# Optimization experiments

Measured on AMD Instinct MI355X. Metric: run time of the kernel, lower is better.

The kernel has to match this reference:

```python
import jax, jax.numpy as jnp
import numpy as np

D = 64            # packed days (admission nodes)
VD = 4525         # drug vocab per day
VL = 753          # labitem vocab per day
ND, NLN = D * VD, D * VL
H = 128           # h_dim
EMB = 10          # embedding_size
TV = 100          # token-field vocab size
NH, HD = 8, 16    # attention heads, head dim
L_ENC, FF = 6, 2048
GL = 2            # gnn layers
ED, ET = 32768, 131072  # did / took edge counts
K = 256           # candidates per day


def setup_inputs():
    key = jax.random.key(0)
    ks = iter(jax.random.split(key, 80))
    nk = lambda: next(ks)
    w = lambda *s: 0.02 * jax.random.normal(nk(), s, jnp.float32)
    ones_zeros = jnp.tile(jnp.stack([jnp.ones(H), jnp.zeros(H)])[None], (L_ENC, 1, 1))
    inp = {
        'drug_tokens': jax.random.randint(nk(), (ND, 3), 0, TV),
        'drug_node_id': jax.random.randint(nk(), (ND,), 0, VD),
        'drug_floats': jax.random.normal(nk(), (ND, 2), jnp.float32),
        'lab_tokens': jax.random.randint(nk(), (NLN, 2), 0, TV),
        'lab_node_id': jax.random.randint(nk(), (NLN,), 0, VL),
        'lab_floats': jax.random.normal(nk(), (NLN, 1), jnp.float32),
        'adm_tokens': jax.random.randint(nk(), (D, 4), 0, TV),
        'adm_floats': jax.random.normal(nk(), (D, 3), jnp.float32),
        'did_tokens': jax.random.randint(nk(), (ED, 2), 0, TV),
        'did_floats': jax.random.normal(nk(), (ED, 2), jnp.float32),
        'did_src': jax.random.randint(nk(), (ED,), 0, D),
        'did_dst': jax.random.randint(nk(), (ED,), 0, NLN),
        'took_tokens': jax.random.randint(nk(), (ET, 2), 0, TV),
        'took_floats': jax.random.normal(nk(), (ET, 1), jnp.float32),
        'took_src': jax.random.randint(nk(), (ET,), 0, D),
        'took_dst': jax.random.randint(nk(), (ET,), 0, ND),
        'cand_idx': jax.random.randint(nk(), (D - 1, K), 0, VD),
        # learned parameters (normal std=0.02 as in _init_weights)
        'drug_id_emb': w(VD, EMB), 'lab_id_emb': w(VL, EMB),
        'drug_tok_emb': w(3, TV, EMB), 'lab_tok_emb': w(2, TV, EMB),
        'adm_tok_emb': w(4, TV, EMB),
        'did_tok_emb': w(2, TV, EMB), 'took_tok_emb': w(2, TV, EMB),
        'drug_float_w': w(2, EMB), 'lab_float_w': w(1, EMB), 'adm_float_w': w(3, EMB),
        'did_float_w': w(2, EMB), 'took_float_w': w(1, EMB),
        'drug_align': w(5 * EMB, H), 'lab_align': w(4 * EMB, H), 'adm_align': w(5 * EMB, H),
        'did_align': w(3 * EMB, H), 'took_align': w(3 * EMB, H),
        'gnn_w_msg': w(GL, 4, H, H), 'gnn_w_self': w(GL, 3, H, H),
        'tr_qkv_w': w(L_ENC, H, 3 * H), 'tr_qkv_b': jnp.zeros((L_ENC, 3 * H), jnp.float32),
        'tr_out_w': w(L_ENC, H, H), 'tr_out_b': jnp.zeros((L_ENC, H), jnp.float32),
        'tr_ln1': ones_zeros,
        'tr_ff1_w': w(L_ENC, H, FF), 'tr_ff1_b': jnp.zeros((L_ENC, FF), jnp.float32),
        'tr_ff2_w': w(L_ENC, FF, H), 'tr_ff2_b': jnp.zeros((L_ENC, H), jnp.float32),
        'tr_ln2': ones_zeros,
        'lp_w': w(H),
    }
    return inp


def _graph_embed(tokens, floats, tok_emb, float_w):
    # per-field token embedding lookup + one slot from float fields -> [N, n_tok+1, EMB]
    nf = tok_emb.shape[0]
    te = tok_emb[jnp.arange(nf), tokens]
    fe = (floats @ float_w)[:, None, :]
    return jnp.concatenate([te, fe], axis=1)


def _seg_mean(msgs, idx, n):
    s = jax.ops.segment_sum(msgs, idx, num_segments=n)
    c = jax.ops.segment_sum(jnp.ones((msgs.shape[0],), msgs.dtype), idx, num_segments=n)
    return s / jnp.maximum(c, 1.0)[:, None]


def _ln(x, sb):
    mu = x.mean(-1, keepdims=True)
    var = ((x - mu) ** 2).mean(-1, keepdims=True)
    return sb[0] * (x - mu) * jax.lax.rsqrt(var + 1e-5) + sb[1]


def _forward(fl, it):
    (drug_floats, lab_floats, adm_floats, did_floats, took_floats,
     drug_id_emb, lab_id_emb, drug_tok_emb, lab_tok_emb, adm_tok_emb,
     did_tok_emb, took_tok_emb, drug_float_w, lab_float_w, adm_float_w,
     did_float_w, took_float_w, drug_align, lab_align, adm_align,
     did_align, took_align, gnn_w_msg, gnn_w_self,
     tr_qkv_w, tr_qkv_b, tr_out_w, tr_out_b, tr_ln1,
     tr_ff1_w, tr_ff1_b, tr_ff2_w, tr_ff2_b, tr_ln2, lp_w) = fl
    (drug_tokens, drug_node_id, lab_tokens, lab_node_id, adm_tokens,
     did_tokens, took_tokens, did_src, did_dst, took_src, took_dst, cand_idx) = it
    # per-type embed + concat(id, fields) + align (LazyLinear, no bias)
    x_d = jnp.concatenate([drug_id_emb[drug_node_id][:, None, :],
                           _graph_embed(drug_tokens, drug_floats, drug_tok_emb, drug_float_w)], 1)
    x_d = x_d.reshape(ND, -1) @ drug_align
    x_l = jnp.concatenate([lab_id_emb[lab_node_id][:, None, :],
                           _graph_embed(lab_tokens, lab_floats, lab_tok_emb, lab_float_w)], 1)
    x_l = x_l.reshape(NLN, -1) @ lab_align
    x_a = _graph_embed(adm_tokens, adm_floats, adm_tok_emb, adm_float_w).reshape(D, -1) @ adm_align
    e_did = _graph_embed(did_tokens, did_floats, did_tok_emb, did_float_w).reshape(ED, -1) @ did_align
    e_took = _graph_embed(took_tokens, took_floats, took_tok_emb, took_float_w).reshape(ET, -1) @ took_align
    # hetero message passing (to_hetero: per-edge-type conv, sum over incoming types)
    for l in range(GL):
        m_l = _seg_mean((x_a[did_src] + e_did) @ gnn_w_msg[l, 0], did_dst, NLN)
        m_d = _seg_mean((x_a[took_src] + e_took) @ gnn_w_msg[l, 1], took_dst, ND)
        m_a = (_seg_mean((x_l[did_dst] + e_did) @ gnn_w_msg[l, 2], did_src, D)
               + _seg_mean((x_d[took_dst] + e_took) @ gnn_w_msg[l, 3], took_src, D))
        x_a = x_a @ gnn_w_self[l, 0] + m_a
        x_d = x_d @ gnn_w_self[l, 1] + m_d
        x_l = x_l @ gnn_w_self[l, 2] + m_l
        if l < GL - 1:
            x_a, x_d, x_l = jax.nn.relu(x_a), jax.nn.relu(x_d), jax.nn.relu(x_l)
    # causal transformer encoder over per-day admission states (torch post-LN, relu)
    mask = jnp.where(jnp.tril(jnp.ones((D, D), bool)), 0.0, -1e9)
    h = x_a
    for i in range(L_ENC):
        q, k, v = jnp.split(h @ tr_qkv_w[i] + tr_qkv_b[i], 3, axis=-1)
        q = q.reshape(D, NH, HD); k = k.reshape(D, NH, HD); v = v.reshape(D, NH, HD)
        att = jax.nn.softmax(jnp.einsum('qhd,khd->hqk', q, k) * 0.25 + mask, axis=-1)
        o = jnp.einsum('hqk,khd->qhd', att, v).reshape(D, H) @ tr_out_w[i] + tr_out_b[i]
        h = _ln(h + o, tr_ln1[i])
        f = jax.nn.relu(h @ tr_ff1_w[i] + tr_ff1_b[i]) @ tr_ff2_w[i] + tr_ff2_b[i]
        h = _ln(h + f, tr_ln2[i])
    # link prediction: prev-day patient state vs candidate item embeddings
    drug_day = x_d.reshape(D, VD, H)
    items = drug_day[jnp.arange(D - 1)[:, None], cand_idx]  # [D-1, K, H]
    logits = jnp.einsum('dkh,dh,h->dk', items, h[:D - 1], lp_w)
    return logits


def reference(drug_floats, lab_floats, adm_floats, did_floats, took_floats,
              drug_id_emb, lab_id_emb, drug_tok_emb, lab_tok_emb, adm_tok_emb,
              did_tok_emb, took_tok_emb, drug_float_w, lab_float_w, adm_float_w,
              did_float_w, took_float_w, drug_align, lab_align, adm_align,
              did_align, took_align, gnn_w_msg, gnn_w_self,
              tr_qkv_w, tr_qkv_b, tr_out_w, tr_out_b, tr_ln1,
              tr_ff1_w, tr_ff1_b, tr_ff2_w, tr_ff2_b, tr_ln2, lp_w,
              drug_tokens, drug_node_id, lab_tokens, lab_node_id, adm_tokens,
              did_tokens, took_tokens, did_src, did_dst, took_src, took_dst, cand_idx):
    fl = (drug_floats, lab_floats, adm_floats, did_floats, took_floats,
          drug_id_emb, lab_id_emb, drug_tok_emb, lab_tok_emb, adm_tok_emb,
          did_tok_emb, took_tok_emb, drug_float_w, lab_float_w, adm_float_w,
          did_float_w, took_float_w, drug_align, lab_align, adm_align,
          did_align, took_align, gnn_w_msg, gnn_w_self,
          tr_qkv_w, tr_qkv_b, tr_out_w, tr_out_b, tr_ln1,
          tr_ff1_w, tr_ff1_b, tr_ff2_w, tr_ff2_b, tr_ln2, lp_w)
    it = (drug_tokens, drug_node_id, lab_tokens, lab_node_id, adm_tokens,
          did_tokens, took_tokens, did_src, did_dst, took_src, took_dst, cand_idx)
    return _forward(fl, it)
```

## Files before the change

### kernel.cpp

```cpp
#include <hip/hip_runtime.h>
#include <hip/hip_bf16.h>

typedef unsigned short ushort_t;
typedef unsigned long long u64;
typedef __attribute__((ext_vector_type(8))) short bf16x8;
typedef __attribute__((ext_vector_type(4))) float f32x4;

#define DEV __device__ __forceinline__

constexpr int Dd  = 64;
constexpr int VD  = 4525;
constexpr int VL  = 753;
constexpr int ND  = Dd * VD;
constexpr int NLN = Dd * VL;
constexpr int Hh  = 128;
constexpr int EMB = 10;
constexpr int TV  = 100;
constexpr int NH  = 8, HD = 16;
constexpr int L_ENC = 6, FF = 2048;
constexpr int GL  = 2;
constexpr int ED  = 32768, ET = 131072;
constexpr int KK  = 256;
constexpr int NCAND = (Dd - 1) * KK;
constexpr int UCAP  = ET + NCAND;
// ... 16 lines not shown
{
    int tid = threadIdx.x;
    int c = 0;
    #pragma unroll
    for (int i = 0; i < 16; i++) c += (w[tid * 16 + i] >> 14) & 1;
    #pragma unroll
    for (int o = 32; o; o >>= 1) c += __shfl_xor(c, o);
    if (tid == 0) *flag = (c > 256) ? 1 : 0;
}

struct CanonDesc {
    const void* src[NCANON];
    int doff[NCANON];
    int bend[NCANON];
    int n[NCANON];
};

__global__ __launch_bounds__(256)
void k_canon(CanonDesc cd, float* __restrict__ dst, const int* __restrict__ flag)
{
    int b = blockIdx.x;
    int t = 0;
    while (t < NCANON && b >= cd.bend[t]) t++;
    if (t >= NCANON) return;
    int bstart = (t == 0) ? 0 : cd.bend[t - 1];
    int i = (b - bstart) * 256 + threadIdx.x;
    if (i >= cd.n[t]) return;
    float v = (*flag) ? ((const float*)cd.src[t])[i]
                      : bf(((const ushort_t*)cd.src[t])[i]);
    dst[cd.doff[t] + i] = v;
}

__global__ __launch_bounds__(128)
void k_wpack(const float* __restrict__ gself, const float* __restrict__ gmsg,
             ushort_t* __restrict__ wt)
{
    const int selfIdx[3] = {1, 2, 4};
    const int msgIdx[3]  = {1, 0, 5};
    int pr = blockIdx.y, chunk = blockIdx.x, nn = threadIdx.x;
    const float* Ws = gself + (size_t)selfIdx[pr] * Hh * Hh;
    const float* Wm = gmsg  + (size_t)msgIdx[pr]  * Hh * Hh;
    ushort_t* dst = wt + (((size_t)pr * 32 + chunk) * 128 + nn) * 8;
    #pragma unroll
    for (int j = 0; j < 8; j++) {
        int k = chunk * 8 + j;
        float v = (k < 128) ? Ws[k * Hh + nn] : Wm[(k - 128) * Hh + nn];
        dst[j] = f2bf(v);
    }
}

__global__ __launch_bounds__(128)
void k_apack(const float* __restrict__ A, ushort_t* __restrict__ dst, int L)
{
    int c = blockIdx.x, nn = threadIdx.x;
    ushort_t* d = dst + ((size_t)c * 128 + nn) * 8;
    #pragma unroll
    for (int j = 0; j < 8; j++) {
        int k = c * 8 + j;
        d[j] = (k < L) ? f2bf(A[(size_t)k * Hh + nn]) : (ushort_t)0;
    }
}

__global__ __launch_bounds__(256)
void k_mark(const int* __restrict__ took_dst, const int* __restrict__ cand,
            int* __restrict__ map)
{
    int g = blockIdx.x * 256 + threadIdx.x;
    if (g < ET) atomicOr(&map[took_dst[g]], 1);
    if (g < NCAND) {
        int d = g >> 8;
        atomicOr(&map[d * VD + cand[g]], 2);
    }
}

__global__ __launch_bounds__(256)
void k_acount(const int* __restrict__ map, u64* __restrict__ bsum)
{
    __shared__ u64 s[256];
    int tid = threadIdx.x;
    int g = blockIdx.x * 256 + tid;
    int m = (g < ND) ? map[g] : 0;
    s[tid] = (u64)(m ? 1u : 0u) | ((u64)((m & 2) ? 1u : 0u) << 32);
    __syncthreads();
    for (int o = 128; o; o >>= 1) {
        if (tid < o) s[tid] += s[tid + o];
        __syncthreads();
    }
    if (tid == 0) bsum[blockIdx.x] = s[0];
}

__global__ __launch_bounds__(1024)
void k_ascan(u64* __restrict__ bsum, int nb, int* __restrict__ nUB)
// ... 50 lines not shown
}

__global__ __launch_bounds__(256)
void k_counts(const int* __restrict__ did_dst, const int* __restrict__ did_src,
              const int* __restrict__ took_dst, const int* __restrict__ took_src,
              const int* __restrict__ map,
              int* __restrict__ cnt_ld, int* __restrict__ cnt_a1,
              int* __restrict__ cnt_dc, int* __restrict__ cnt_a2)
{
    __shared__ int h1[64], h2[64];
    int tid = threadIdx.x;
    if (tid < 64) { h1[tid] = 0; h2[tid] = 0; }
    __syncthreads();
    int tb = blockIdx.x * 1024;
    #pragma unroll
    for (int o = 0; o < 1024; o += 256) {
        int i = tb + o + tid;
        atomicAdd(&cnt_dc[map[took_dst[i]] >> 2], 1);
        atomicAdd(&h2[took_src[i]], 1);
    }
    {
        int i = blockIdx.x * 256 + tid;
        atomicAdd(&cnt_ld[did_dst[i]], 1);
        atomicAdd(&h1[did_src[i]], 1);
    }
    __syncthreads();
    if (tid < 64) {
        if (h1[tid]) atomicAdd(&cnt_a1[tid], h1[tid]);
        if (h2[tid]) atomicAdd(&cnt_a2[tid], h2[tid]);
    }
}

__global__ __launch_bounds__(256)
void k_scan_blk(const int* __restrict__ cnt, int* __restrict__ excl,
                int* __restrict__ btot, int n)
{
    __shared__ int s[256];
    int tid = threadIdx.x;
    int g = blockIdx.x * 256 + tid;
    int v = (g < n) ? cnt[g] : 0;
    s[tid] = v;
    __syncthreads();
    for (int o = 1; o < 256; o <<= 1) {
        int t = (tid >= o) ? s[tid - o] : 0;
        __syncthreads();
        s[tid] += t;
        __syncthreads();
    }
    if (g < n) excl[g] = s[tid] - v;
    if (tid == 255) btot[blockIdx.x] = s[255];
}

__global__ __launch_bounds__(1024)
void k_scan_top(int* __restrict__ btot, int nb)
{
    __shared__ int s[1024];
    int tid = threadIdx.x;
    int v = (tid < nb) ? btot[tid] : 0;
    s[tid] = v;
    __syncthreads();
    for (int o = 1; o < 1024; o <<= 1) {
        int t = (tid >= o) ? s[tid - o] : 0;
        __syncthreads();
        s[tid] += t;
        __syncthreads();
    }
    if (tid < nb) btot[tid] = s[tid] - v;
}

__global__ __launch_bounds__(256)
void k_scan_add(int* __restrict__ roff, const int* __restrict__ btot, int n, int total)
{
    int g = blockIdx.x * 256 + threadIdx.x;
    if (g < n) roff[g] += btot[blockIdx.x];
    if (g == 0) roff[n] = total;
}

__global__ __launch_bounds__(64)
void k_scan64(const int* __restrict__ c1, const int* __restrict__ c2,
              int* __restrict__ r1, int* __restrict__ r2)
{
    int tid = threadIdx.x;
    int v1 = c1[tid], v2 = c2[tid];
    int s1 = v1, s2 = v2;
    for (int o = 1; o < 64; o <<= 1) {
        int t1 = __shfl_up(s1, o), t2 = __shfl_up(s2, o);
        if (tid >= o) { s1 += t1; s2 += t2; }
    }
    r1[tid] = s1 - v1;
    r2[tid] = s2 - v2;
}

__global__ __launch_bounds__(256)
void k_fill(const int* __restrict__ did_src, const int* __restrict__ did_dst,
            const int* __restrict__ took_src, const int* __restrict__ took_dst,
            const int* __restrict__ map,
            const int* __restrict__ roff_d, const int* __restrict__ roff_t,
            const int* __restrict__ roff_a1, const int* __restrict__ roff_a2,
            int* __restrict__ cur_d, int* __restrict__ cur_t,
            int* __restrict__ cur_a1, int* __restrict__ cur_a2,
            int* __restrict__ elist_d, int* __restrict__ elist_t,
            int* __restrict__ didA, int* __restrict__ didB,
            int* __restrict__ tookA, int* __restrict__ tookB)
{
    __shared__ int h1[64], h2[64], b1[64], b2[64];
    int tid = threadIdx.x;
    if (tid < 64) { h1[tid] = 0; h2[tid] = 0; }
    __syncthreads();
    int tb = blockIdx.x * 1024;
    int db = blockIdx.x * 256;
    #pragma unroll
    for (int o = 0; o < 1024; o += 256)
        atomicAdd(&h2[took_src[tb + o + tid]], 1);
    atomicAdd(&h1[did_src[db + tid]], 1);
    __syncthreads();
    if (tid < 64) {
        b1[tid] = h1[tid] ? atomicAdd(&cur_a1[tid], h1[tid]) : 0;
        b2[tid] = h2[tid] ? atomicAdd(&cur_a2[tid], h2[tid]) : 0;
        h1[tid] = 0; h2[tid] = 0;
    }
    __syncthreads();
    #pragma unroll
    for (int o = 0; o < 1024; o += 256) {
// ... 163 lines not shown
    }
    __syncthreads();
    float* Ds = reinterpret_cast<float*>(As);
    #pragma unroll
    for (int nt = 0; nt < 8; nt++)
        #pragma unroll
        for (int reg = 0; reg < 4; reg++)
            Ds[(16 * wid + quad * 4 + reg) * 132 + nt * 16 + m] = acc[nt][reg];
    __syncthreads();
    for (int idx = tid; idx < 512; idx += 128) {
        int r = idx >> 4, c16 = idx & 15;
        int slot = r0 + r;
        if (slot >= n) continue;
        const float* dsrc = &Ds[r * 132 + c16 * 8];
        uint4 v;
        v.x = (unsigned)f2bf(dsrc[0]) | ((unsigned)f2bf(dsrc[1]) << 16);
        v.y = (unsigned)f2bf(dsrc[2]) | ((unsigned)f2bf(dsrc[3]) << 16);
        v.z = (unsigned)f2bf(dsrc[4]) | ((unsigned)f2bf(dsrc[5]) << 16);
        v.w = (unsigned)f2bf(dsrc[6]) | ((unsigned)f2bf(dsrc[7]) << 16);
        *reinterpret_cast<uint4*>(out + (size_t)slot * Hh + c16 * 8) = v;
    }
}

template<bool INDIRECT>
__global__ __launch_bounds__(128)
void k_gup(ushort_t* __restrict__ X, const float* __restrict__ xa,
           const ushort_t* __restrict__ ef,
           const int* __restrict__ roff, const int* __restrict__ elist, int sshift,
           const int* __restrict__ rows_list, const int* __restrict__ n_dyn, int n_static,
           const ushort_t* __restrict__ Wt, int do_relu)
{
    __shared__ ushort_t As[32 * 264];
    __shared__ int rowid[32];
    int tid = threadIdx.x;
    int r0 = blockIdx.x * 32;
    int n = n_dyn ? *n_dyn : n_static;
    if (tid < 32) {
        int row = r0 + tid;
        rowid[tid] = (row < n) ? (INDIRECT ? rows_list[row] : row) : -1;
    }
    __syncthreads();

    for (int idx = tid; idx < 512; idx += 128) {
        int r = idx >> 4, c16 = idx & 15;
        int rr = rowid[r];
        uint4 v = make_uint4(0, 0, 0, 0);
        if (rr >= 0) v = *reinterpret_cast<const uint4*>(X + (size_t)rr * Hh + c16 * 8);
        *reinterpret_cast<uint4*>(&As[r * 264 + c16 * 8]) = v;
    }
    int wid = tid >> 6, lane = tid & 63;
    int c0 = lane * 2;
    int emask = (1 << sshift) - 1;
    for (int r = wid; r < 32; r += 2) {
        int rr = rowid[r];
        float a0 = 0.f, a1 = 0.f, invd = 0.f;
        if (rr >= 0) {
            int e0 = roff[rr], e1 = roff[rr + 1];
            invd = 1.f / fmaxf((float)(e1 - e0), 1.f);
            for (int ei = e0; ei < e1; ei++) {
                int pk = elist[ei];
                int s = pk >> sshift, e = pk & emask;
                const float* xr = xa + s * Hh + c0;
                unsigned ee = *reinterpret_cast<const unsigned*>(ef + (size_t)e * Hh + c0);
                a0 += xr[0] + bflo(ee);
                a1 += xr[1] + bfhi(ee);
            }
        }
        unsigned pk2 = (unsigned)f2bf(a0 * invd) | ((unsigned)f2bf(a1 * invd) << 16);
        *reinterpret_cast<unsigned*>(&As[r * 264 + 128 + c0]) = pk2;
    }
    __syncthreads();

    int m = lane & 15, quad = lane >> 4;
    f32x4 acc[8];
    #pragma unroll
    for (int t = 0; t < 8; t++) acc[t] = (f32x4){0.f, 0.f, 0.f, 0.f};
    #pragma unroll
    for (int kc = 0; kc < 8; kc++) {
        bf16x8 a = *reinterpret_cast<const bf16x8*>(&As[(16 * wid + m) * 264 + kc * 32 + quad * 8]);
        #pragma unroll
        for (int nt = 0; nt < 8; nt++) {
            bf16x8 b = *reinterpret_cast<const bf16x8*>(Wt + (((kc * 4 + quad) * 128) + nt * 16 + m) * 8);
            acc[nt] = __builtin_amdgcn_mfma_f32_16x16x32_bf16(a, b, acc[nt], 0, 0, 0);
        }
    }
    __syncthreads();
    float* Ds = reinterpret_cast<float*>(As);
    #pragma unroll
    for (int nt = 0; nt < 8; nt++)
        #pragma unroll
        for (int reg = 0; reg < 4; reg++)
            Ds[(16 * wid + quad * 4 + reg) * 132 + nt * 16 + m] = acc[nt][reg];
    __syncthreads();
// ... 13 lines not shown
        v.y = (unsigned)f2bf(o[2]) | ((unsigned)f2bf(o[3]) << 16);
        v.z = (unsigned)f2bf(o[4]) | ((unsigned)f2bf(o[5]) << 16);
        v.w = (unsigned)f2bf(o[6]) | ((unsigned)f2bf(o[7]) << 16);
        *reinterpret_cast<uint4*>(X + (size_t)rr * Hh + c16 * 8) = v;
    }
}

__global__ __launch_bounds__(128)
void k_xa(float* __restrict__ x_a,
          const float* __restrict__ Sx1, const float* __restrict__ E1,
          const float* __restrict__ Sx2, const float* __restrict__ E2,
          const int* __restrict__ c1, const int* __restrict__ c2,
          const float* __restrict__ Wself, const float* __restrict__ Wm1,
          const float* __restrict__ Wm2, int do_relu)
{
    int r = blockIdx.x, tid = threadIdx.x;
    __shared__ float xr[128], a1[128], a2[128];
    float i1 = 1.f / fmaxf((float)c1[r], 1.f);
    float i2 = 1.f / fmaxf((float)c2[r], 1.f);
    xr[tid] = x_a[r * Hh + tid];
    a1[tid] = (Sx1[r * Hh + tid] + E1[r * Hh + tid]) * i1;
    a2[tid] = (Sx2[r * Hh + tid] + E2[r * Hh + tid]) * i2;
    __syncthreads();
    float acc = 0.f;
    for (int k = 0; k < 128; k++) {
        acc = fmaf(xr[k], Wself[k * Hh + tid], acc);
        acc = fmaf(a1[k], Wm1[k * Hh + tid], acc);
        acc = fmaf(a2[k], Wm2[k * Hh + tid], acc);
    }
    if (do_relu) acc = fmaxf(acc, 0.f);
    x_a[r * Hh + tid] = acc;
}

__global__ __launch_bounds__(128)
void k_qkv3(const float* __restrict__ h, float* __restrict__ qkv,
            const float* __restrict__ W, const float* __restrict__ b)
{
    int r = blockIdx.x, part = blockIdx.y, tid = threadIdx.x;
    int c = part * 128 + tid;
    __shared__ float hr[128];
    hr[tid] = h[r * Hh + tid];
    __syncthreads();
    float a0 = b[c], a1 = 0.f, a2 = 0.f, a3 = 0.f;
    for (int k = 0; k < 128; k += 4) {
        a0 = fmaf(hr[k],     W[(k)     * 384 + c], a0);
        a1 = fmaf(hr[k + 1], W[(k + 1) * 384 + c], a1);
        a2 = fmaf(hr[k + 2], W[(k + 2) * 384 + c], a2);
        a3 = fmaf(hr[k + 3], W[(k + 3) * 384 + c], a3);
    }
    qkv[r * 384 + c] = (a0 + a1) + (a2 + a3);
}

__global__ __launch_bounds__(64)
void k_attn2(const float* __restrict__ qkv, float* __restrict__ attn_o)
{
    int hh = blockIdx.x, q = blockIdx.y;
    int lane = threadIdx.x;
    const float* qv = qkv + q * 384 + hh * HD;
    const float* kv = qkv + lane * 384 + 128 + hh * HD;
    float s = 0.f;
    #pragma unroll
    for (int d2 = 0; d2 < HD; d2++) s = fmaf(qv[d2], kv[d2], s);
    s = s * 0.25f + (lane <= q ? 0.f : -1e9f);
    float m = s;
    #pragma unroll
    for (int o = 32; o; o >>= 1) m = fmaxf(m, __shfl_xor(m, o));
    float e = __expf(s - m);
    float tot = e;
    #pragma unroll
    for (int o = 32; o; o >>= 1) tot += __shfl_xor(tot, o);
    float att = e / tot;
    __shared__ float satt[64];
    satt[lane] = att;
    __syncthreads();
    if (lane < HD) {
        float o0 = 0.f, o1 = 0.f, o2 = 0.f, o3 = 0.f;
        for (int k2 = 0; k2 < Dd; k2 += 4) {
            o0 = fmaf(satt[k2],     qkv[(k2)     * 384 + 256 + hh * HD + lane], o0);
            o1 = fmaf(satt[k2 + 1], qkv[(k2 + 1) * 384 + 256 + hh * HD + lane], o1);
            o2 = fmaf(satt[k2 + 2], qkv[(k2 + 2) * 384 + 256 + hh * HD + lane], o2);
            o3 = fmaf(satt[k2 + 3], qkv[(k2 + 3) * 384 + 256 + hh * HD + lane], o3);
        }
        attn_o[q * Hh + hh * HD + lane] = (o0 + o1) + (o2 + o3);
    }
}

DEV float blocksum128(float v, float* red)
{
    #pragma unroll
    for (int o = 32; o; o >>= 1) v += __shfl_xor(v, o);
    int wid = threadIdx.x >> 6;
    __syncthreads();
    if ((threadIdx.x & 63) == 0) red[wid] = v;
    __syncthreads();
    return red[0] + red[1];
}

__global__ __launch_bounds__(128)
void k_outln(const float* __restrict__ attn_o, float* __restrict__ h,
             const float* __restrict__ Wout, const float* __restrict__ bout,
             const float* __restrict__ ln)
{
    int r = blockIdx.x, tid = threadIdx.x;
    __shared__ float ar[128];
    __shared__ float red[2];
    ar[tid] = attn_o[r * Hh + tid];
    __syncthreads();
    float a0 = bout[tid], a1 = 0.f, a2 = 0.f, a3 = 0.f;
    for (int k = 0; k < 128; k += 4) {
        a0 = fmaf(ar[k],     Wout[(k)     * Hh + tid], a0);
        a1 = fmaf(ar[k + 1], Wout[(k + 1) * Hh + tid], a1);
        a2 = fmaf(ar[k + 2], Wout[(k + 2) * Hh + tid], a2);
        a3 = fmaf(ar[k + 3], Wout[(k + 3) * Hh + tid], a3);
    }
    float x = h[r * Hh + tid] + (a0 + a1) + (a2 + a3);
    float mu = blocksum128(x, red) * (1.f / 128.f);
    float dx = x - mu;
    float var = blocksum128(dx * dx, red) * (1.f / 128.f);
    h[r * Hh + tid] = ln[tid] * dx * (1.f / sqrtf(var + 1e-5f)) + ln[128 + tid];
}

__global__ __launch_bounds__(256)
void k_ff1b(const float* __restrict__ h, float* __restrict__ fbuf,
            const float* __restrict__ W1, const float* __restrict__ b1)
{
    int r = blockIdx.x, tid = threadIdx.x;
    int c = blockIdx.y * 256 + tid;
    __shared__ float hr[128];
    if (tid < 128) hr[tid] = h[r * Hh + tid];
    __syncthreads();
    float a0 = b1[c], a1 = 0.f, a2 = 0.f, a3 = 0.f;
    for (int k = 0; k < 128; k += 4) {
        a0 = fmaf(hr[k],     W1[(size_t)(k)     * FF + c], a0);
        a1 = fmaf(hr[k + 1], W1[(size_t)(k + 1) * FF + c], a1);
        a2 = fmaf(hr[k + 2], W1[(size_t)(k + 2) * FF + c], a2);
        a3 = fmaf(hr[k + 3], W1[(size_t)(k + 3) * FF + c], a3);
    }
    fbuf[(size_t)r * FF + c] = fmaxf((a0 + a1) + (a2 + a3), 0.f);
}

__global__ __launch_bounds__(128)
void k_ff2p(const float* __restrict__ fbuf, float* __restrict__ part,
            const float* __restrict__ W2)
{
    int r = blockIdx.x, pi = blockIdx.y, tid = threadIdx.x;
    int kc = pi * 128;
    const float* f = fbuf + (size_t)r * FF + kc;
    float a0 = 0.f, a1 = 0.f, a2 = 0.f, a3 = 0.f;
    for (int k = 0; k < 128; k += 4) {
        a0 = fmaf(f[k],     W2[(size_t)(kc + k)     * Hh + tid], a0);
        a1 = fmaf(f[k + 1], W2[(size_t)(kc + k + 1) * Hh + tid], a1);
        a2 = fmaf(f[k + 2], W2[(size_t)(kc + k + 2) * Hh + tid], a2);
        a3 = fmaf(f[k + 3], W2[(size_t)(kc + k + 3) * Hh + tid], a3);
    }
    part[(size_t)(r * 16 + pi) * Hh + tid] = (a0 + a1) + (a2 + a3);
}

__global__ __launch_bounds__(128)
void k_ln2(float* __restrict__ h, const float* __restrict__ part,
           const float* __restrict__ b2, const float* __restrict__ ln)
{
    int r = blockIdx.x, tid = threadIdx.x;
    __shared__ float red[2];
    float acc = b2[tid];
    #pragma unroll
    for (int pi = 0; pi < 16; pi++) acc += part[(size_t)(r * 16 + pi) * Hh + tid];
    float x = h[r * Hh + tid] + acc;
    float mu = blocksum128(x, red) * (1.f / 128.f);
    float dx = x - mu;
    float var = blocksum128(dx * dx, red) * (1.f / 128.f);
    h[r * Hh + tid] = ln[tid] * dx * (1.f / sqrtf(var + 1e-5f)) + ln[128 + tid];
}

__global__ __launch_bounds__(256)
void k_logits(const ushort_t* __restrict__ x_dc, const int* __restrict__ map,
              const float* __restrict__ h, const float* __restrict__ lp,
              const int* __restrict__ cand, float* __restrict__ out)
{
    int d = blockIdx.x;
    int tid = threadIdx.x, lane = tid & 63, w = tid >> 6;
    __shared__ float wv[128];
    if (tid < 128) wv[tid] = h[d * Hh + tid] * lp[tid];
    __syncthreads();
    for (int k = w; k < KK; k += 4) {
        int slot = map[d * VD + cand[d * KK + k]] >> 2;
        const ushort_t* row = x_dc + (size_t)slot * Hh;
        float v = bf(row[lane]) * wv[lane] + bf(row[lane + 64]) * wv[lane + 64];
        #pragma unroll
// ... 44 lines not shown
            cd.doff[t] = e;
            e = (e + cn[t] + 7) & ~7;
            btot_blocks += (cn[t] + 255) / 256;
            cd.bend[t] = btot_blocks;
        }
        eoff[NCANON] = e;
    }

    char* p = (char*)d_ws;
    auto alloc_f = [&](size_t n) -> float*    { float* r = (float*)p;    p += n * sizeof(float); return r; };
    auto alloc_h = [&](size_t n) -> ushort_t* { ushort_t* r = (ushort_t*)p; p += n * sizeof(ushort_t); return r; };
    auto alloc_i = [&](size_t n) -> int*      { int* r = (int*)p;        p += n * sizeof(int); return r; };

    int* map    = alloc_i(ND);
    int* cnt_dc = alloc_i(UCAP);
    int* cnt_ld = alloc_i(NLN);
    int* cnt_a1 = alloc_i(64);
    int* cnt_a2 = alloc_i(64);
    int* nUB    = alloc_i(8);
    int* cur_t  = alloc_i(UCAP);
    int* cur_d  = alloc_i(NLN);
    int* cur_a1 = alloc_i(64);
    int* cur_a2 = alloc_i(64);
    float* E_did  = alloc_f((size_t)Dd * Hh);
    float* E_took = alloc_f((size_t)Dd * Hh);
    const size_t ZBLOCK = (size_t)ND + UCAP + NLN + 64 + 64 + 8 + UCAP + NLN + 64 + 64
                        + (size_t)Dd * Hh * 2;
    float* Sx_did  = alloc_f((size_t)Dd * Hh);
    float* Sx_took = alloc_f((size_t)Dd * Hh);
    int* roff_t  = alloc_i(UCAP + 8);
    int* roff_d  = alloc_i(NLN + 8);
    int* roff_a1 = alloc_i(72);
    int* roff_a2 = alloc_i(72);
    int* bscr    = alloc_i(1024);
    u64* absum   = (u64*)alloc_i(2 * (NB_A + 8));
    int* ulist   = alloc_i(UCAP);
    int* blist   = alloc_i(NCAND);
    int* elist_t = alloc_i(ET);
    int* elist_d = alloc_i(ED);
    int* tookA   = alloc_i(ET);
    int* tookB   = alloc_i(ET);
    int* didA    = alloc_i(ED);
    int* didB    = alloc_i(ED);
    ushort_t* wt     = alloc_h(3 * 32768);
    ushort_t* ap     = alloc_h(2 * 8192 + 2 * 4096);
    ushort_t* x_dc   = alloc_h((size_t)UCAP * Hh);
    ushort_t* x_l    = alloc_h((size_t)NLN * Hh);
    float*    x_a    = alloc_f((size_t)Dd * Hh);
    ushort_t* e_did  = alloc_h((size_t)ED * Hh);
    ushort_t* e_took = alloc_h((size_t)ET * Hh);
    float*    qkvb   = alloc_f((size_t)Dd * 384);
    float*    attn_o = alloc_f((size_t)Dd * Hh);
    float*    fbuf   = alloc_f((size_t)Dd * FF);
    float*    part   = alloc_f((size_t)Dd * 16 * Hh);
    float*    cf     = alloc_f((size_t)eoff[NCANON]);
    int*      dflag  = alloc_i(8);

    ushort_t* ap_drug = ap;
    ushort_t* ap_lab  = ap + 8192;
    ushort_t* ap_did  = ap + 16384;
    ushort_t* ap_took = ap + 16384 + 4096;

    const float* c_drug_floats  = cf + eoff[0];
    const float* c_lab_floats   = cf + eoff[1];
    const float* c_adm_floats   = cf + eoff[2];
    const float* c_did_floats   = cf + eoff[3];
    const float* c_took_floats  = cf + eoff[4];
    const float* c_drug_id_emb  = cf + eoff[5];
    const float* c_lab_id_emb   = cf + eoff[6];
    const float* c_drug_tok_emb = cf + eoff[7];
    const float* c_lab_tok_emb  = cf + eoff[8];
    const float* c_adm_tok_emb  = cf + eoff[9];
    const float* c_did_tok_emb  = cf + eoff[10];
    const float* c_took_tok_emb = cf + eoff[11];
    const float* c_drug_float_w = cf + eoff[12];
    const float* c_lab_float_w  = cf + eoff[13];
    const float* c_adm_float_w  = cf + eoff[14];
    const float* c_did_float_w  = cf + eoff[15];
    const float* c_took_float_w = cf + eoff[16];
    const float* c_drug_align   = cf + eoff[17];
    const float* c_lab_align    = cf + eoff[18];
    const float* c_adm_align    = cf + eoff[19];
    const float* c_did_align    = cf + eoff[20];
    const float* c_took_align   = cf + eoff[21];
    const float* c_gnn_msg      = cf + eoff[22];
    const float* c_gnn_self     = cf + eoff[23];
    const float* c_qkv_w        = cf + eoff[24];
    const float* c_qkv_b        = cf + eoff[25];
    const float* c_out_w        = cf + eoff[26];
    const float* c_out_b        = cf + eoff[27];
    const float* c_ln1          = cf + eoff[28];
    const float* c_ff1_w        = cf + eoff[29];
    const float* c_ff1_b        = cf + eoff[30];
    const float* c_ff2_w        = cf + eoff[31];
    const float* c_ff2_b        = cf + eoff[32];
    const float* c_ln2          = cf + eoff[33];
    const float* c_lp_w         = cf + eoff[34];

    k_probe<<<1, 64, 0, stream>>>((const unsigned*)d_in[41], dflag);
    k_canon<<<btot_blocks, 256, 0, stream>>>(cd, cf, dflag);
    k_wpack<<<dim3(32, 3), 128, 0, stream>>>(c_gnn_self, c_gnn_msg, wt);
    k_apack<<<8, 128, 0, stream>>>(c_drug_align, ap_drug, 50);
    k_apack<<<8, 128, 0, stream>>>(c_lab_align,  ap_lab,  40);
    k_apack<<<4, 128, 0, stream>>>(c_did_align,  ap_did,  30);
    k_apack<<<4, 128, 0, stream>>>(c_took_align, ap_took, 30);
    hipMemsetAsync(map, 0, ZBLOCK * sizeof(int), stream);
    k_mark<<<ET / 256, 256, 0, stream>>>(took_dst, cand_idx, map);
    k_acount<<<NB_A, 256, 0, stream>>>(map, absum);
    k_ascan<<<1, 1024, 0, stream>>>(absum, NB_A, nUB);
    k_assign2<<<NB_A, 256, 0, stream>>>(map, ulist, blist, absum);
    k_counts<<<128, 256, 0, stream>>>(did_dst, did_src, took_dst, took_src, map,
                                      cnt_ld, cnt_a1, cnt_dc, cnt_a2);
    k_scan_blk<<<NB_T, 256, 0, stream>>>(cnt_dc, roff_t, bscr, UCAP);
    k_scan_top<<<1, 1024, 0, stream>>>(bscr, NB_T);
    k_scan_add<<<NB_T, 256, 0, stream>>>(roff_t, bscr, UCAP, ET);
    k_scan_blk<<<NB_D, 256, 0, stream>>>(cnt_ld, roff_d, bscr, NLN);
    k_scan_top<<<1, 1024, 0, stream>>>(bscr, NB_D);
    k_scan_add<<<NB_D, 256, 0, stream>>>(roff_d, bscr, NLN, ED);
    k_scan64<<<1, 64, 0, stream>>>(cnt_a1, cnt_a2, roff_a1, roff_a2);
    k_fill<<<128, 256, 0, stream>>>(did_src, did_dst, took_src, took_dst, map,
                                    roff_d, roff_t, roff_a1, roff_a2,
                                    cur_d, cur_t, cur_a1, cur_a2,
                                    elist_d, elist_t, didA, didB, tookA, tookB);

    k_embed_m<1,3,2,2,true><<<UCAP / 32, 128, 0, stream>>>(x_dc, 0, nUB, ulist,
        drug_node_id, c_drug_id_emb, drug_tokens, c_drug_tok_emb,
        c_drug_floats, c_drug_float_w, ap_drug);
    k_embed_m<1,2,1,2,false><<<NLN / 32, 128, 0, stream>>>(x_l, NLN, nullptr, nullptr,
        lab_node_id, c_lab_id_emb, lab_tokens, c_lab_tok_emb,
        c_lab_floats, c_lab_float_w, ap_lab);
    k_embed_adm<<<Dd, 128, 0, stream>>>(x_a, adm_tokens, c_adm_tok_emb,
                                        c_adm_floats, c_adm_float_w, c_adm_align);
    k_embed_m<0,2,2,1,false><<<ED / 32, 128, 0, stream>>>(e_did, ED, nullptr, nullptr,
        nullptr, nullptr, did_tokens, c_did_tok_emb, c_did_floats, c_did_float_w, ap_did);
    k_embed_m<0,2,1,1,false><<<ET / 32, 128, 0, stream>>>(e_took, ET, nullptr, nullptr,
        nullptr, nullptr, took_tokens, c_took_tok_emb, c_took_floats, c_took_float_w, ap_took);

    const size_t HH = (size_t)Hh * Hh;

    hipMemsetAsync(Sx_did, 0, 2 * (size_t)Dd * Hh * sizeof(float), stream);
    k_srcsum<true><<<(ED + 31) / 32, 64, 0, stream>>>(didA, didB, x_l, e_did, 16,
                                                      Sx_did, E_did, ED, 32);
    k_srcsum<true><<<(ET + 31) / 32, 64, 0, stream>>>(tookA, tookB, x_dc, e_took, 18,
                                                      Sx_took, E_took, ET, 32);
    k_gup<false><<<UCAP / 32, 128, 0, stream>>>(x_dc, x_a, e_took, roff_t, elist_t, 17,
        nullptr, nUB, 0, wt, 1);
    k_gup<false><<<NLN / 32, 128, 0, stream>>>(x_l, x_a, e_did, roff_d, elist_d, 15,
        nullptr, nullptr, NLN, wt + 32768, 1);
    k_xa<<<Dd, 128, 0, stream>>>(x_a, Sx_did, E_did, Sx_took, E_took, cnt_a1, cnt_a2,
        c_gnn_self + 0 * HH, c_gnn_msg + 2 * HH, c_gnn_msg + 3 * HH, 1);

    const float* Ws1 = c_gnn_self + 3 * HH;
    const float* Wm1 = c_gnn_msg + 4 * HH;
    hipMemsetAsync(Sx_did, 0, 2 * (size_t)Dd * Hh * sizeof(float), stream);
    k_srcsum<false><<<(ED + 31) / 32, 64, 0, stream>>>(didA, didB, x_l, nullptr, 16,
                                                       Sx_did, nullptr, ED, 32);
    k_srcsum<false><<<(ET + 31) / 32, 64, 0, stream>>>(tookA, tookB, x_dc, nullptr, 18,
                                                       Sx_took, nullptr, ET, 32);
    k_gup<true><<<(NCAND + 31) / 32, 128, 0, stream>>>(x_dc, x_a, e_took, roff_t, elist_t, 17,
        blist, nUB + 1, 0, wt + 65536, 0);
    k_xa<<<Dd, 128, 0, stream>>>(x_a, Sx_did, E_did, Sx_took, E_took, cnt_a1, cnt_a2,
        Ws1 + 0 * HH, Wm1 + 2 * HH, Wm1 + 3 * HH, 0);

    for (int i = 0; i < L_ENC; i++) {
        k_qkv3<<<dim3(Dd, 3), 128, 0, stream>>>(x_a, qkvb,
            c_qkv_w + (size_t)i * Hh * 384, c_qkv_b + (size_t)i * 384);
        k_attn2<<<dim3(NH, Dd), 64, 0, stream>>>(qkvb, attn_o);
        k_outln<<<Dd, 128, 0, stream>>>(attn_o, x_a, c_out_w + (size_t)i * HH,
                                        c_out_b + (size_t)i * Hh, c_ln1 + (size_t)i * 2 * Hh);
        k_ff1b<<<dim3(Dd, FF / 256), 256, 0, stream>>>(x_a, fbuf,
            c_ff1_w + (size_t)i * Hh * FF, c_ff1_b + (size_t)i * FF);
        k_ff2p<<<dim3(Dd, 16), 128, 0, stream>>>(fbuf, part, c_ff2_w + (size_t)i * FF * Hh);
        k_ln2<<<Dd, 128, 0, stream>>>(x_a, part, c_ff2_b + (size_t)i * Hh,
                                      c_ln2 + (size_t)i * 2 * Hh);
    }

    k_logits<<<Dd - 1, 256, 0, stream>>>(x_dc, map, x_a, c_lp_w, cand_idx, (float*)d_out);
}
```

Measured before the change: 729.7 us.

## Fuse small kernels and stage edge lists in shared memory

```diff
diff --git a/kernel.cpp b/kernel.cpp
--- a/kernel.cpp
+++ b/kernel.cpp
@@ -72,32 +72,38 @@
 }
 
 __global__ __launch_bounds__(128)
-void k_wpack(const float* __restrict__ gself, const float* __restrict__ gmsg,
-             ushort_t* __restrict__ wt)
-{
-    const int selfIdx[3] = {1, 2, 4};
-    const int msgIdx[3]  = {1, 0, 5};
-    int pr = blockIdx.y, chunk = blockIdx.x, nn = threadIdx.x;
-    const float* Ws = gself + (size_t)selfIdx[pr] * Hh * Hh;
-    const float* Wm = gmsg  + (size_t)msgIdx[pr]  * Hh * Hh;
-    ushort_t* dst = wt + (((size_t)pr * 32 + chunk) * 128 + nn) * 8;
-    #pragma unroll
-    for (int j = 0; j < 8; j++) {
-        int k = chunk * 8 + j;
-        float v = (k < 128) ? Ws[k * Hh + nn] : Wm[(k - 128) * Hh + nn];
-        dst[j] = f2bf(v);
-    }
-}
-
-__global__ __launch_bounds__(128)
-void k_apack(const float* __restrict__ A, ushort_t* __restrict__ dst, int L)
-{
-    int c = blockIdx.x, nn = threadIdx.x;
-    ushort_t* d = dst + ((size_t)c * 128 + nn) * 8;
-    #pragma unroll
-    for (int j = 0; j < 8; j++) {
-        int k = c * 8 + j;
-        d[j] = (k < L) ? f2bf(A[(size_t)k * Hh + nn]) : (ushort_t)0;
+void k_packall(const float* __restrict__ gself, const float* __restrict__ gmsg,
+               const float* __restrict__ a_drug, const float* __restrict__ a_lab,
+               const float* __restrict__ a_did, const float* __restrict__ a_took,
+               ushort_t* __restrict__ wt, ushort_t* __restrict__ ap)
+{
+    int sel = blockIdx.y, chunk = blockIdx.x, nn = threadIdx.x;
+    if (sel < 3) {
+        const int selfIdx[3] = {1, 2, 4};
+        const int msgIdx[3]  = {1, 0, 5};
+        const float* Ws = gself + (size_t)selfIdx[sel] * Hh * Hh;
+        const float* Wm = gmsg  + (size_t)msgIdx[sel]  * Hh * Hh;
+        ushort_t* dst = wt + (((size_t)sel * 32 + chunk) * 128 + nn) * 8;
+        #pragma unroll
+        for (int j = 0; j < 8; j++) {
+            int k = chunk * 8 + j;
+            float v = (k < 128) ? Ws[k * Hh + nn] : Wm[(k - 128) * Hh + nn];
+            dst[j] = f2bf(v);
+        }
+    } else {
+        int ai = sel - 3;
+        const int nchunk[4] = {8, 8, 4, 4};
+        if (chunk >= nchunk[ai]) return;
+        const int Ls[4] = {50, 40, 30, 30};
+        const int aoff[4] = {0, 8192, 16384, 16384 + 4096};
+        const float* A = (ai == 0) ? a_drug : (ai == 1) ? a_lab : (ai == 2) ? a_did : a_took;
+        ushort_t* d = ap + aoff[ai] + ((size_t)chunk * 128 + nn) * 8;
+        int L = Ls[ai];
+        #pragma unroll
+        for (int j = 0; j < 8; j++) {
+            int k = chunk * 8 + j;
+            d[j] = (k < L) ? f2bf(A[(size_t)k * Hh + nn]) : (ushort_t)0;
+        }
     }
 }
 
@@ -214,12 +220,16 @@
 }
 
 __global__ __launch_bounds__(256)
-void k_scan_blk(const int* __restrict__ cnt, int* __restrict__ excl,
-                int* __restrict__ btot, int n)
+void k_scan_blk2(const int* __restrict__ cnt_dc, int* __restrict__ roff_t,
+                 const int* __restrict__ cnt_ld, int* __restrict__ roff_d,
+                 int* __restrict__ bscrT, int* __restrict__ bscrD)
 {
     __shared__ int s[256];
     int tid = threadIdx.x;
-    int g = blockIdx.x * 256 + tid;
+    const int* cnt; int* excl; int* btot; int n; int blk;
+    if (blockIdx.x < NB_T) { cnt = cnt_dc; excl = roff_t; btot = bscrT; n = UCAP; blk = blockIdx.x; }
+    else { cnt = cnt_ld; excl = roff_d; btot = bscrD; n = NLN; blk = blockIdx.x - NB_T; }
+    int g = blk * 256 + tid;
     int v = (g < n) ? cnt[g] : 0;
     s[tid] = v;
     __syncthreads();
@@ -230,14 +240,31 @@
         __syncthreads();
     }
     if (g < n) excl[g] = s[tid] - v;
-    if (tid == 255) btot[blockIdx.x] = s[255];
+    if (tid == 255) btot[blk] = s[255];
 }
 
 __global__ __launch_bounds__(1024)
-void k_scan_top(int* __restrict__ btot, int nb)
-{
+void k_scan_top2(int* __restrict__ bscrT, int* __restrict__ bscrD,
+                 const int* __restrict__ c1, const int* __restrict__ c2,
+                 int* __restrict__ r1, int* __restrict__ r2)
+{
+    int tid = threadIdx.x;
+    if (blockIdx.x == 2) {
+        if (tid < 64) {
+            int v1 = c1[tid], v2 = c2[tid];
+            int s1 = v1, s2 = v2;
+            for (int o = 1; o < 64; o <<= 1) {
+                int t1 = __shfl_up(s1, o), t2 = __shfl_up(s2, o);
+                if (tid >= o) { s1 += t1; s2 += t2; }
+            }
+            r1[tid] = s1 - v1;
+            r2[tid] = s2 - v2;
+        }
+        return;
+    }
     __shared__ int s[1024];
-    int tid = threadIdx.x;
+    int* btot = (blockIdx.x == 0) ? bscrT : bscrD;
+    int nb = (blockIdx.x == 0) ? NB_T : NB_D;
     int v = (tid < nb) ? btot[tid] : 0;
     s[tid] = v;
     __syncthreads();
@@ -251,26 +278,20 @@
 }
 
 __global__ __launch_bounds__(256)
-void k_scan_add(int* __restrict__ roff, const int* __restrict__ btot, int n, int total)
-{
-    int g = blockIdx.x * 256 + threadIdx.x;
-    if (g < n) roff[g] += btot[blockIdx.x];
-    if (g == 0) roff[n] = total;
-}
-
-__global__ __launch_bounds__(64)
-void k_scan64(const int* __restrict__ c1, const int* __restrict__ c2,
-              int* __restrict__ r1, int* __restrict__ r2)
+void k_scan_add2(int* __restrict__ roff_t, const int* __restrict__ bscrT,
+                 int* __restrict__ roff_d, const int* __restrict__ bscrD)
 {
     int tid = threadIdx.x;
-    int v1 = c1[tid], v2 = c2[tid];
-    int s1 = v1, s2 = v2;
-    for (int o = 1; o < 64; o <<= 1) {
-        int t1 = __shfl_up(s1, o), t2 = __shfl_up(s2, o);
-        if (tid >= o) { s1 += t1; s2 += t2; }
-    }
-    r1[tid] = s1 - v1;
-    r2[tid] = s2 - v2;
+    if (blockIdx.x < NB_T) {
+        int g = blockIdx.x * 256 + tid;
+        if (g < UCAP) roff_t[g] += bscrT[blockIdx.x];
+        if (g == 0) roff_t[UCAP] = ET;
+    } else {
+        int blk = blockIdx.x - NB_T;
+        int g = blk * 256 + tid;
+        if (g < NLN) roff_d[g] += bscrD[blk];
+        if (g == 0) roff_d[NLN] = ED;
+    }
 }
 
 __global__ __launch_bounds__(256)
@@ -500,6 +521,8 @@
 {
     __shared__ ushort_t As[32 * 264];
     __shared__ int rowid[32];
+    __shared__ int off[33];
+    __shared__ int el[1024];
     int tid = threadIdx.x;
     int r0 = blockIdx.x * 32;
     int n = n_dyn ? *n_dyn : n_static;
@@ -507,6 +530,7 @@
         int row = r0 + tid;
         rowid[tid] = (row < n) ? (INDIRECT ? rows_list[row] : row) : -1;
     }
+    if (!INDIRECT && tid < 33) off[tid] = roff[r0 + tid];
     __syncthreads();
 
     for (int idx = tid; idx < 512; idx += 128) {
@@ -516,6 +540,16 @@
         if (rr >= 0) v = *reinterpret_cast<const uint4*>(X + (size_t)rr * Hh + c16 * 8);
         *reinterpret_cast<uint4*>(&As[r * 264 + c16 * 8]) = v;
     }
+    int eb = 0, ne = 0;
+    bool fast = false;
+    if (!INDIRECT) {
+        eb = off[0];
+        ne = off[32] - eb;
+        fast = (ne <= 1024);
+        if (fast) for (int j = tid; j < ne; j += 128) el[j] = elist[eb + j];
+    }
+    __syncthreads();
+
     int wid = tid >> 6, lane = tid & 63;
     int c0 = lane * 2;
     int emask = (1 << sshift) - 1;
@@ -523,10 +557,12 @@
         int rr = rowid[r];
         float a0 = 0.f, a1 = 0.f, invd = 0.f;
         if (rr >= 0) {
-            int e0 = roff[rr], e1 = roff[rr + 1];
+            int e0, e1;
+            if (!INDIRECT) { e0 = off[r]; e1 = off[r + 1]; }
+            else { e0 = roff[rr]; e1 = roff[rr + 1]; }
             invd = 1.f / fmaxf((float)(e1 - e0), 1.f);
             for (int ei = e0; ei < e1; ei++) {
-                int pk = elist[ei];
+                int pk = (!INDIRECT && fast) ? el[ei - eb] : elist[ei];
                 int s = pk >> sshift, e = pk & emask;
                 const float* xr = xa + s * Hh + c0;
                 unsigned ee = *reinterpret_cast<const unsigned*>(ef + (size_t)e * Hh + c0);
@@ -606,6 +642,28 @@
     x_a[r * Hh + tid] = acc;
 }
 
+DEV float blocksum128(float v, float* red)
+{
+    #pragma unroll
+    for (int o = 32; o; o >>= 1) v += __shfl_xor(v, o);
+    int wid = threadIdx.x >> 6;
+    __syncthreads();
+    if ((threadIdx.x & 63) == 0) red[wid] = v;
+    __syncthreads();
+    return red[0] + red[1];
+}
+
+DEV float blocksum256(float v, float* red)
+{
+    #pragma unroll
+    for (int o = 32; o; o >>= 1) v += __shfl_xor(v, o);
+    int wid = threadIdx.x >> 6;
+    __syncthreads();
+    if ((threadIdx.x & 63) == 0) red[wid] = v;
+    __syncthreads();
+    return red[0] + red[1] + red[2] + red[3];
+}
+
 __global__ __launch_bounds__(128)
 void k_qkv3(const float* __restrict__ h, float* __restrict__ qkv,
             const float* __restrict__ W, const float* __restrict__ b)
@@ -659,50 +717,40 @@
     }
 }
 
-DEV float blocksum128(float v, float* red)
-{
-    #pragma unroll
-    for (int o = 32; o; o >>= 1) v += __shfl_xor(v, o);
-    int wid = threadIdx.x >> 6;
-    __syncthreads();
-    if ((threadIdx.x & 63) == 0) red[wid] = v;
-    __syncthreads();
-    return red[0] + red[1];
-}
-
-__global__ __launch_bounds__(128)
-void k_outln(const float* __restrict__ attn_o, float* __restrict__ h,
+__global__ __launch_bounds__(256)
+void k_outff(const float* __restrict__ attn_o, float* __restrict__ h,
+             float* __restrict__ fbuf,
              const float* __restrict__ Wout, const float* __restrict__ bout,
-             const float* __restrict__ ln)
+             const float* __restrict__ ln,
+             const float* __restrict__ W1, const float* __restrict__ b1)
 {
     int r = blockIdx.x, tid = threadIdx.x;
     __shared__ float ar[128];
-    __shared__ float red[2];
-    ar[tid] = attn_o[r * Hh + tid];
-    __syncthreads();
-    float a0 = bout[tid], a1 = 0.f, a2 = 0.f, a3 = 0.f;
-    for (int k = 0; k < 128; k += 4) {
-        a0 = fmaf(ar[k],     Wout[(k)     * Hh + tid], a0);
-        a1 = fmaf(ar[k + 1], Wout[(k + 1) * Hh + tid], a1);
-        a2 = fmaf(ar[k + 2], Wout[(k + 2) * Hh + tid], a2);
-        a3 = fmaf(ar[k + 3], Wout[(k + 3) * Hh + tid], a3);
-    }
-    float x = h[r * Hh + tid] + (a0 + a1) + (a2 + a3);
-    float mu = blocksum128(x, red) * (1.f / 128.f);
-    float dx = x - mu;
-    float var = blocksum128(dx * dx, red) * (1.f / 128.f);
-    h[r * Hh + tid] = ln[tid] * dx * (1.f / sqrtf(var + 1e-5f)) + ln[128 + tid];
-}
-
-__global__ __launch_bounds__(256)
-void k_ff1b(const float* __restrict__ h, float* __restrict__ fbuf,
-            const float* __restrict__ W1, const float* __restrict__ b1)
-{
-    int r = blockIdx.x, tid = threadIdx.x;
+    __shared__ float hr[128];
+    __shared__ float red[4];
+    if (tid < 128) ar[tid] = attn_o[r * Hh + tid];
+    __syncthreads();
+    float x = 0.f;
+    if (tid < 128) {
+        float a0 = bout[tid], a1 = 0.f, a2 = 0.f, a3 = 0.f;
+        for (int k = 0; k < 128; k += 4) {
+            a0 = fmaf(ar[k],     Wout[(k)     * Hh + tid], a0);
+            a1 = fmaf(ar[k + 1], Wout[(k + 1) * Hh + tid], a1);
+            a2 = fmaf(ar[k + 2], Wout[(k + 2) * Hh + tid], a2);
+            a3 = fmaf(ar[k + 3], Wout[(k + 3) * Hh + tid], a3);
+        }
+        x = h[r * Hh + tid] + (a0 + a1) + (a2 + a3);
+    }
+    float mu = blocksum256(x, red) * (1.f / 128.f);
+    float dx = (tid < 128) ? (x - mu) : 0.f;
+    float var = blocksum256(dx * dx, red) * (1.f / 128.f);
+    if (tid < 128) {
+        float y = ln[tid] * dx * (1.f / sqrtf(var + 1e-5f)) + ln[128 + tid];
+        hr[tid] = y;
+        if (blockIdx.y == 0) h[r * Hh + tid] = y;
+    }
+    __syncthreads();
     int c = blockIdx.y * 256 + tid;
-    __shared__ float hr[128];
-    if (tid < 128) hr[tid] = h[r * Hh + tid];
-    __syncthreads();
     float a0 = b1[c], a1 = 0.f, a2 = 0.f, a3 = 0.f;
     for (int k = 0; k < 128; k += 4) {
         a0 = fmaf(hr[k],     W1[(size_t)(k)     * FF + c], a0);
@@ -728,6 +776,37 @@
         a3 = fmaf(f[k + 3], W2[(size_t)(kc + k + 3) * Hh + tid], a3);
     }
     part[(size_t)(r * 16 + pi) * Hh + tid] = (a0 + a1) + (a2 + a3);
+}
+
+__global__ __launch_bounds__(128)
+void k_ln2qkv3(float* __restrict__ h, const float* __restrict__ part,
+               const float* __restrict__ b2, const float* __restrict__ ln,
+               float* __restrict__ qkv, const float* __restrict__ Wq,
+               const float* __restrict__ bq)
+{
+    int r = blockIdx.x, pid = blockIdx.y, tid = threadIdx.x;
+    __shared__ float red[2];
+    __shared__ float hr[128];
+    float acc = b2[tid];
+    #pragma unroll
+    for (int pi = 0; pi < 16; pi++) acc += part[(size_t)(r * 16 + pi) * Hh + tid];
+    float x = h[r * Hh + tid] + acc;
+    float mu = blocksum128(x, red) * (1.f / 128.f);
+    float dx = x - mu;
+    float var = blocksum128(dx * dx, red) * (1.f / 128.f);
+    float y = ln[tid] * dx * (1.f / sqrtf(var + 1e-5f)) + ln[128 + tid];
+    hr[tid] = y;
+    if (pid == 0) h[r * Hh + tid] = y;
+    __syncthreads();
+    int c = pid * 128 + tid;
+    float a0 = bq[c], a1 = 0.f, a2 = 0.f, a3 = 0.f;
+    for (int k = 0; k < 128; k += 4) {
+        a0 = fmaf(hr[k],     Wq[(k)     * 384 + c], a0);
+        a1 = fmaf(hr[k + 1], Wq[(k + 1) * 384 + c], a1);
+        a2 = fmaf(hr[k + 2], Wq[(k + 2) * 384 + c], a2);
+        a3 = fmaf(hr[k + 3], Wq[(k + 3) * 384 + c], a3);
+    }
+    qkv[r * 384 + c] = (a0 + a1) + (a2 + a3);
 }
 
 __global__ __launch_bounds__(128)
@@ -838,7 +917,7 @@
     int* roff_d  = alloc_i(NLN + 8);
     int* roff_a1 = alloc_i(72);
     int* roff_a2 = alloc_i(72);
-    int* bscr    = alloc_i(1024);
+    int* bscr    = alloc_i(2048);
     u64* absum   = (u64*)alloc_i(2 * (NB_A + 8));
     int* ulist   = alloc_i(UCAP);
     int* blist   = alloc_i(NCAND);
@@ -862,6 +941,8 @@
     float*    cf     = alloc_f((size_t)eoff[NCANON]);
     int*      dflag  = alloc_i(8);
 
+    int* bscrT = bscr;
+    int* bscrD = bscr + 1024;
     ushort_t* ap_drug = ap;
     ushort_t* ap_lab  = ap + 8192;
     ushort_t* ap_did  = ap + 16384;
@@ -905,11 +986,8 @@
 
     k_probe<<<1, 64, 0, stream>>>((const unsigned*)d_in[41], dflag);
     k_canon<<<btot_blocks, 256, 0, stream>>>(cd, cf, dflag);
-    k_wpack<<<dim3(32, 3), 128, 0, stream>>>(c_gnn_self, c_gnn_msg, wt);
-    k_apack<<<8, 128, 0, stream>>>(c_drug_align, ap_drug, 50);
-    k_apack<<<8, 128, 0, stream>>>(c_lab_align,  ap_lab,  40);
-    k_apack<<<4, 128, 0, stream>>>(c_did_align,  ap_did,  30);
-    k_apack<<<4, 128, 0, stream>>>(c_took_align, ap_took, 30);
+    k_packall<<<dim3(32, 7), 128, 0, stream>>>(c_gnn_self, c_gnn_msg,
+        c_drug_align, c_lab_align, c_did_align, c_took_align, wt, ap);
     hipMemsetAsync(map, 0, ZBLOCK * sizeof(int), stream);
     k_mark<<<ET / 256, 256, 0, stream>>>(took_dst, cand_idx, map);
     k_acount<<<NB_A, 256, 0, stream>>>(map, absum);
@@ -917,13 +995,9 @@
     k_assign2<<<NB_A, 256, 0, stream>>>(map, ulist, blist, absum);
     k_counts<<<128, 256, 0, stream>>>(did_dst, did_src, took_dst, took_src, map,
                                       cnt_ld, cnt_a1, cnt_dc, cnt_a2);
-    k_scan_blk<<<NB_T, 256, 0, stream>>>(cnt_dc, roff_t, bscr, UCAP);
-    k_scan_top<<<1, 1024, 0, stream>>>(bscr, NB_T);
-    k_scan_add<<<NB_T, 256, 0, stream>>>(roff_t, bscr, UCAP, ET);
-    k_scan_blk<<<NB_D, 256, 0, stream>>>(cnt_ld, roff_d, bscr, NLN);
-    k_scan_top<<<1, 1024, 0, stream>>>(bscr, NB_D);
-    k_scan_add<<<NB_D, 256, 0, stream>>>(roff_d, bscr, NLN, ED);
-    k_scan64<<<1, 64, 0, stream>>>(cnt_a1, cnt_a2, roff_a1, roff_a2);
+    k_scan_blk2<<<NB_T + NB_D, 256, 0, stream>>>(cnt_dc, roff_t, cnt_ld, roff_d, bscrT, bscrD);
+    k_scan_top2<<<3, 1024, 0, stream>>>(bscrT, bscrD, cnt_a1, cnt_a2, roff_a1, roff_a2);
+    k_scan_add2<<<NB_T + NB_D, 256, 0, stream>>>(roff_t, bscrT, roff_d, bscrD);
     k_fill<<<128, 256, 0, stream>>>(did_src, did_dst, took_src, took_dst, map,
                                     roff_d, roff_t, roff_a1, roff_a2,
                                     cur_d, cur_t, cur_a1, cur_a2,
@@ -968,17 +1042,21 @@
     k_xa<<<Dd, 128, 0, stream>>>(x_a, Sx_did, E_did, Sx_took, E_took, cnt_a1, cnt_a2,
         Ws1 + 0 * HH, Wm1 + 2 * HH, Wm1 + 3 * HH, 0);
 
+    k_qkv3<<<dim3(Dd, 3), 128, 0, stream>>>(x_a, qkvb, c_qkv_w, c_qkv_b);
     for (int i = 0; i < L_ENC; i++) {
-        k_qkv3<<<dim3(Dd, 3), 128, 0, stream>>>(x_a, qkvb,
-            c_qkv_w + (size_t)i * Hh * 384, c_qkv_b + (size_t)i * 384);
         k_attn2<<<dim3(NH, Dd), 64, 0, stream>>>(qkvb, attn_o);
-        k_outln<<<Dd, 128, 0, stream>>>(attn_o, x_a, c_out_w + (size_t)i * HH,
-                                        c_out_b + (size_t)i * Hh, c_ln1 + (size_t)i * 2 * Hh);
-        k_ff1b<<<dim3(Dd, FF / 256), 256, 0, stream>>>(x_a, fbuf,
+        k_outff<<<dim3(Dd, 8), 256, 0, stream>>>(attn_o, x_a, fbuf,
+            c_out_w + (size_t)i * HH, c_out_b + (size_t)i * Hh, c_ln1 + (size_t)i * 2 * Hh,
             c_ff1_w + (size_t)i * Hh * FF, c_ff1_b + (size_t)i * FF);
         k_ff2p<<<dim3(Dd, 16), 128, 0, stream>>>(fbuf, part, c_ff2_w + (size_t)i * FF * Hh);
-        k_ln2<<<Dd, 128, 0, stream>>>(x_a, part, c_ff2_b + (size_t)i * Hh,
-                                      c_ln2 + (size_t)i * 2 * Hh);
+        if (i + 1 < L_ENC) {
+            k_ln2qkv3<<<dim3(Dd, 3), 128, 0, stream>>>(x_a, part,
+                c_ff2_b + (size_t)i * Hh, c_ln2 + (size_t)i * 2 * Hh, qkvb,
+                c_qkv_w + (size_t)(i + 1) * Hh * 384, c_qkv_b + (size_t)(i + 1) * 384);
+        } else {
+            k_ln2<<<Dd, 128, 0, stream>>>(x_a, part, c_ff2_b + (size_t)i * Hh,
+                                          c_ln2 + (size_t)i * 2 * Hh);
+        }
     }
 
     k_logits<<<Dd - 1, 256, 0, stream>>>(x_dc, map, x_a, c_lp_w, cand_idx, (float*)d_out);
```

Measured after the change: 674.3 us. 1.08x faster.
